# Performance work log

Hardware: AMD Instinct MI355X
Metric: run time of the kernel (lower is better)

Reference implementation:

```python
import jax, jax.numpy as jnp
import numpy as np

B, N, D = 256, 2048, 256

def setup_inputs() -> dict:
    key = jax.random.key(0)
    k1, k2, k3, k4 = jax.random.split(key, 4)
    feature = jax.random.normal(k1, (B, N, D), dtype=jnp.float32)
    pointer_hidden_state = jax.random.normal(k2, (B, D), dtype=jnp.float32)
    # learned params (match torch.randn init)
    v = jax.random.normal(k3, (1, 1, D), dtype=jnp.float32)
    W = jax.random.normal(k4, (1, D, 2 * D), dtype=jnp.float32)
    return {"feature": feature, "pointer_hidden_state": pointer_hidden_state, "v": v, "W": W}

def reference(feature, pointer_hidden_state, v, W):
    # hidden: concat(feature, broadcast hidden state) -> [B, N, 2D]
    b, n, d = feature.shape
    h = jnp.broadcast_to(pointer_hidden_state[:, None, :], (b, n, d))
    hidden = jnp.concatenate([feature, h], axis=2)            # [B, N, 2D]
    # W @ hidden^T fused as einsum: [D, 2D] x [B, N, 2D] -> [B, N, D]
    pre = jnp.tanh(jnp.einsum('de,bne->bnd', W[0], hidden))
    # v . pre -> [B, N]
    scores = jnp.einsum('d,bnd->bn', v[0, 0], pre)
    attns = jax.nn.softmax(scores, axis=1)[:, None, :]        # [B, 1, N]
    return attns
```

## Files before the change

kernel.cpp:

```cpp
#include <hip/hip_runtime.h>
#include <hip/hip_fp16.h>

typedef _Float16 f16;
typedef _Float16 f16x4 __attribute__((ext_vector_type(4)));
typedef _Float16 f16x8 __attribute__((ext_vector_type(8)));
typedef float f32x4 __attribute__((ext_vector_type(4)));

#define NCH 64
#define CHB 32768
#define PLB 16384
#define PSTRIDE 524288

#define BAR()     asm volatile("s_waitcnt lgkmcnt(0)\n\ts_barrier" ::: "memory")
#define WAITV_(N) asm volatile("s_waitcnt vmcnt(" #N ")" ::: "memory")
#define WAITV(N)  WAITV_(N)

__global__ void prep_w(const float* __restrict__ W, f16* __restrict__ wbuf) {
    int idx = blockIdx.x * 256 + threadIdx.x;
    int d = idx >> 8, k = idx & 255;
    float w = W[d * 512 + k];
    int ct   = d >> 4;
    int lane = (d & 15) | (((k >> 3) & 3) << 4);
    int ks   = k >> 5;
    int j    = k & 7;
    wbuf[(((ks * 16 + ct) * 64) + lane) * 8 + j] = (f16)w;
}

__global__ void prep_c(const float* __restrict__ W, const float* __restrict__ h,
                       float* __restrict__ c) {
    __shared__ float hs[256];
    int b = blockIdx.x, d = threadIdx.x;
    hs[d] = h[b * 256 + d];
    __syncthreads();
    const float4* w4 = (const float4*)(W + d * 512 + 256);
    const float4* h4 = (const float4*)hs;
    float acc = 0.f;
#pragma unroll 8
    for (int e = 0; e < 64; ++e) {
        float4 a = w4[e], bb = h4[e];
        acc += a.x * bb.x + a.y * bb.y + a.z * bb.z + a.w * bb.w;
    }
    c[b * 256 + d] = acc;
}

__global__ __launch_bounds__(512, 2)
void main_gemm(const float* __restrict__ feat, const f16* __restrict__ wbuf,
               const float* __restrict__ cb, const float* __restrict__ vvec,
               float* __restrict__ psc) {
    __shared__ __align__(16) char rawb[2 * CHB];
    __shared__ __align__(16) char plnb[2 * PLB];

    const int tid = threadIdx.x;
    const int w = tid >> 6;
    const int l = tid & 63;
    const int g = l >> 4;
    const int lr = l & 15;
    const int rh = w >> 2;
    const int cg = w & 3;
    const int b = blockIdx.x;

    f16x8 wf[4][8];
    {
        const f16x8* wp = (const f16x8*)wbuf;
#pragma unroll
        for (int ct = 0; ct < 4; ++ct) {
            int ctg = cg * 4 + ct;
#pragma unroll
            for (int ks = 0; ks < 8; ++ks)
                wf[ct][ks] = wp[(ks * 16 + ctg) * 64 + l];
        }
    }
    float c_[4], v_[4];
#pragma unroll
    for (int ct = 0; ct < 4; ++ct) {
        c_[ct] = cb[b * 256 + (cg * 4 + ct) * 16 + lr];
        v_[ct] = vvec[(cg * 4 + ct) * 16 + lr];
    }

    const char* tbb = (const char*)(feat + (size_t)b * 2048 * 256);

#define ISSUE(u)                                                                   \
    {                                                                              \
        const char* nb = tbb + (size_t)(u) * CHB;                                  \
        char* Q = rawb + ((u) & 1) * CHB;                                          \
        _Pragma("unroll")                                                          \
        for (int i = 0; i < 4; ++i)                                                \
            __builtin_amdgcn_global_load_lds(                                      \
                (const __attribute__((address_space(1))) void*)(nb + i * 8192 + tid * 16), \
                (__attribute__((address_space(3))) void*)(Q + i * 8192 + tid * 16),\
                16, 0, 0);                                                         \
    }

    const int ck0 = (tid & 63) * 4;
    int cvt_off[4];
#pragma unroll
    for (int r = 0; r < 4; ++r) {
        int row = r * 8 + w;
        cvt_off[r] = (((row * 512 + (ck0 & ~7) * 2) ^ ((row & 7) << 4)) +
                      ((ck0 & 4) << 1));
    }

#define CVT(u)                                                                     \
    {                                                                              \
        const char* rp = rawb + ((u) & 1) * CHB;                                   \
        char* hq = plnb + ((u) & 1) * PLB;                                         \
        _Pragma("unroll")                                                          \
        for (int r = 0; r < 4; ++r) {                                              \
            f32x4 x = *(const f32x4*)(rp + r * 8192 + tid * 16);                   \
            f16x4 hv = {(f16)x[0], (f16)x[1], (f16)x[2], (f16)x[3]};               \
            *(f16x4*)(hq + cvt_off[r]) = hv;                                       \
        }                                                                          \
    }

    const int arow = rh * 16 + lr;
    const int aswz = (arow & 7) << 4;

    ISSUE(0); ISSUE(1);
    WAITV(4);
    CVT(0);

    for (int t = 0; t < NCH; ++t) {
        BAR();
        if (t + 2 < NCH) ISSUE(t + 2);

        const char* hp = plnb + (t & 1) * PLB;
        f32x4 acc[4] = {};
#pragma unroll
        for (int ks = 0; ks < 8; ++ks) {
            int ao = (arow * 512 + ks * 64 + g * 16) ^ aswz;
            f16x8 ahi = *(const f16x8*)(hp + ao);
            acc[0] = __builtin_amdgcn_mfma_f32_16x16x32_f16(ahi, wf[0][ks], acc[0], 0, 0, 0);
            acc[1] = __builtin_amdgcn_mfma_f32_16x16x32_f16(ahi, wf[1][ks], acc[1], 0, 0, 0);
            acc[2] = __builtin_amdgcn_mfma_f32_16x16x32_f16(ahi, wf[2][ks], acc[2], 0, 0, 0);
            acc[3] = __builtin_amdgcn_mfma_f32_16x16x32_f16(ahi, wf[3][ks], acc[3], 0, 0, 0);
        }

        float s[4];
#pragma unroll
        for (int r = 0; r < 4; ++r) {
            float a = 0.f;
#pragma unroll
            for (int ct = 0; ct < 4; ++ct) {
                float x = acc[ct][r] + c_[ct];
                float tnh = 1.f - __fdividef(2.f, __expf(2.f * x) + 1.f);
                a += v_[ct] * tnh;
            }
            s[r] = a;
        }
#pragma unroll
        for (int m = 1; m < 16; m <<= 1) {
            s[0] += __shfl_xor(s[0], m, 64);
            s[1] += __shfl_xor(s[1], m, 64);
            s[2] += __shfl_xor(s[2], m, 64);
            s[3] += __shfl_xor(s[3], m, 64);
        }

        if (t < NCH - 2)      WAITV(4);
        else if (t == NCH - 2) WAITV(0);
        if (t + 1 < NCH) CVT(t + 1);

        if (lr == 0) {
            size_t rowg = (size_t)b * 2048 + t * 32 + rh * 16 + g * 4;
            float4 o = {s[0], s[1], s[2], s[3]};
            *(float4*)(psc + (size_t)cg * PSTRIDE + rowg) = o;
        }
    }
#undef ISSUE
#undef CVT
}

__global__ void softmax_k(const float* __restrict__ psc, float* __restrict__ out) {
    __shared__ float red[16];
    int b = blockIdx.x, tid = threadIdx.x;
    float sc[8];
    float m = -3.4e38f;
#pragma unroll
    for (int q = 0; q < 8; ++q) {
        size_t row = (size_t)b * 2048 + q * 256 + tid;
        sc[q] = (psc[row] + psc[PSTRIDE + row]) +
                (psc[2 * PSTRIDE + row] + psc[3 * PSTRIDE + row]);
        m = fmaxf(m, sc[q]);
    }
#pragma unroll
    for (int d = 1; d < 64; d <<= 1) m = fmaxf(m, __shfl_xor(m, d, 64));
    if ((tid & 63) == 0) red[tid >> 6] = m;
    __syncthreads();
    m = fmaxf(fmaxf(red[0], red[1]), fmaxf(red[2], red[3]));
    float e[8], sum = 0.f;
#pragma unroll
    for (int q = 0; q < 8; ++q) { e[q] = __expf(sc[q] - m); sum += e[q]; }
#pragma unroll
    for (int d = 1; d < 64; d <<= 1) sum += __shfl_xor(sum, d, 64);
    if ((tid & 63) == 0) red[8 + (tid >> 6)] = sum;
    __syncthreads();
    sum = (red[8] + red[9]) + (red[10] + red[11]);
    float inv = __fdividef(1.f, sum);
#pragma unroll
    for (int q = 0; q < 8; ++q)
        out[(size_t)b * 2048 + q * 256 + tid] = e[q] * inv;
}

extern "C" void kernel_launch(void* const* d_in, const int* in_sizes, int n_in,
                              void* d_out, int out_size, void* d_ws, size_t ws_size,
                              hipStream_t stream) {
    const float* feat = (const float*)d_in[0];
    const float* h    = (const float*)d_in[1];
    const float* v    = (const float*)d_in[2];
    const float* W    = (const float*)d_in[3];
    float* out = (float*)d_out;

    f16*   wbuf = (f16*)d_ws;
    float* cbuf = (float*)((char*)d_ws + 131072);
    float* psc  = (float*)((char*)d_ws + 524288);

    prep_w<<<256, 256, 0, stream>>>(W, wbuf);
    prep_c<<<256, 256, 0, stream>>>(W, h, cbuf);
    main_gemm<<<256, 512, 0, stream>>>(feat, wbuf, cbuf, v, psc);
    softmax_k<<<256, 256, 0, stream>>>(psc, out);
}
```

Before: 167.7 us.

## Software-pipeline tanh epilogue and fp16 conversion with MFMA chunk loop

Unrolls the chunk loop by two and double-buffers the accumulators in accA and accB. The tanh/v-dot epilogue and shuffle reduction of the previous chunk, plus the fp32-to-fp16 conversion of the next chunk, are interleaved between the MFMA k-steps of the current chunk. The goal is to hide the transcendental and LDS conversion latency behind matrix-core work. The cost is a second set of accumulators on a kernel that already holds a large register-resident W fragment, so spills or lower occupancy are possible. Score stores now lag one chunk, and the drain steps use adjusted vmcnt waits.

```diff
diff --git a/kernel.cpp b/kernel.cpp
--- a/kernel.cpp
+++ b/kernel.cpp
@@ -81,13 +81,13 @@
 
 #define ISSUE(u)                                                                   \
     {                                                                              \
-        const char* nb = tbb + (size_t)(u) * CHB;                                  \
-        char* Q = rawb + ((u) & 1) * CHB;                                          \
+        const char* nb_ = tbb + (size_t)(u) * CHB;                                 \
+        char* Q_ = rawb + ((u) & 1) * CHB;                                         \
         _Pragma("unroll")                                                          \
-        for (int i = 0; i < 4; ++i)                                                \
+        for (int i_ = 0; i_ < 4; ++i_)                                             \
             __builtin_amdgcn_global_load_lds(                                      \
-                (const __attribute__((address_space(1))) void*)(nb + i * 8192 + tid * 16), \
-                (__attribute__((address_space(3))) void*)(Q + i * 8192 + tid * 16),\
+                (const __attribute__((address_space(1))) void*)(nb_ + i_ * 8192 + tid * 16), \
+                (__attribute__((address_space(3))) void*)(Q_ + i_ * 8192 + tid * 16),\
                 16, 0, 0);                                                         \
     }
 
@@ -100,73 +100,96 @@
                       ((ck0 & 4) << 1));
     }
 
-#define CVT(u)                                                                     \
-    {                                                                              \
-        const char* rp = rawb + ((u) & 1) * CHB;                                   \
-        char* hq = plnb + ((u) & 1) * PLB;                                         \
-        _Pragma("unroll")                                                          \
-        for (int r = 0; r < 4; ++r) {                                              \
-            f32x4 x = *(const f32x4*)(rp + r * 8192 + tid * 16);                   \
-            f16x4 hv = {(f16)x[0], (f16)x[1], (f16)x[2], (f16)x[3]};               \
-            *(f16x4*)(hq + cvt_off[r]) = hv;                                       \
-        }                                                                          \
+#define CVTR(U, R)                                                                 \
+    {                                                                              \
+        const char* rp_ = rawb + ((U) & 1) * CHB;                                  \
+        char* hq_ = plnb + ((U) & 1) * PLB;                                        \
+        f32x4 x_ = *(const f32x4*)(rp_ + (R) * 8192 + tid * 16);                   \
+        f16x4 hv_ = {(f16)x_[0], (f16)x_[1], (f16)x_[2], (f16)x_[3]};              \
+        *(f16x4*)(hq_ + cvt_off[R]) = hv_;                                         \
     }
 
     const int arow = rh * 16 + lr;
     const int aswz = (arow & 7) << 4;
 
+#define KS(KSI, ACC)                                                               \
+    {                                                                              \
+        int ao_ = (arow * 512 + (KSI) * 64 + g * 16) ^ aswz;                       \
+        f16x8 ah_ = *(const f16x8*)(hp_ + ao_);                                    \
+        ACC[0] = __builtin_amdgcn_mfma_f32_16x16x32_f16(ah_, wf[0][KSI], ACC[0], 0, 0, 0); \
+        ACC[1] = __builtin_amdgcn_mfma_f32_16x16x32_f16(ah_, wf[1][KSI], ACC[1], 0, 0, 0); \
+        ACC[2] = __builtin_amdgcn_mfma_f32_16x16x32_f16(ah_, wf[2][KSI], ACC[2], 0, 0, 0); \
+        ACC[3] = __builtin_amdgcn_mfma_f32_16x16x32_f16(ah_, wf[3][KSI], ACC[3], 0, 0, 0); \
+    }
+
+#define EPIS(ACCP, R, SV)                                                          \
+    {                                                                              \
+        float a_ = 0.f;                                                            \
+        _Pragma("unroll")                                                          \
+        for (int ct_ = 0; ct_ < 4; ++ct_) {                                        \
+            float x_ = ACCP[ct_][R] + c_[ct_];                                     \
+            float t_ = 1.f - __fdividef(2.f, __expf(2.f * x_) + 1.f);              \
+            a_ += v_[ct_] * t_;                                                    \
+        }                                                                          \
+        a_ += __shfl_xor(a_, 1, 64);                                               \
+        a_ += __shfl_xor(a_, 2, 64);                                               \
+        a_ += __shfl_xor(a_, 4, 64);                                               \
+        a_ += __shfl_xor(a_, 8, 64);                                               \
+        SV = a_;                                                                   \
+    }
+
+#define STEP(T, ACC, ACCP, DOISS, WS, DOCVT)                                       \
+    {                                                                              \
+        BAR();                                                                     \
+        if (DOISS) ISSUE((T) + 2);                                                 \
+        WS;                                                                        \
+        const char* hp_ = plnb + ((T) & 1) * PLB;                                  \
+        ACC[0] = zf; ACC[1] = zf; ACC[2] = zf; ACC[3] = zf;                        \
+        float sA_, sB_, sC_, sD_;                                                  \
+        KS(0, ACC) if (DOCVT) CVTR((T) + 1, 0)                                     \
+        KS(1, ACC) EPIS(ACCP, 0, sA_)                                              \
+        KS(2, ACC) if (DOCVT) CVTR((T) + 1, 1)                                     \
+        KS(3, ACC) EPIS(ACCP, 1, sB_)                                              \
+        KS(4, ACC) if (DOCVT) CVTR((T) + 1, 2)                                     \
+        KS(5, ACC) EPIS(ACCP, 2, sC_)                                              \
+        KS(6, ACC) if (DOCVT) CVTR((T) + 1, 3)                                     \
+        KS(7, ACC) EPIS(ACCP, 3, sD_)                                              \
+        if ((T) > 0 && lr == 0) {                                                  \
+            size_t rowg = (size_t)b * 2048 + (size_t)((T) - 1) * 32 + rh * 16 + g * 4; \
+            float4 o_ = {sA_, sB_, sC_, sD_};                                      \
+            *(float4*)(psc + (size_t)cg * PSTRIDE + rowg) = o_;                    \
+        }                                                                          \
+    }
+
+    const f32x4 zf = {0.f, 0.f, 0.f, 0.f};
+    f32x4 accA[4] = {zf, zf, zf, zf};
+    f32x4 accB[4] = {zf, zf, zf, zf};
+
     ISSUE(0); ISSUE(1);
     WAITV(4);
-    CVT(0);
-
-    for (int t = 0; t < NCH; ++t) {
-        BAR();
-        if (t + 2 < NCH) ISSUE(t + 2);
-
-        const char* hp = plnb + (t & 1) * PLB;
-        f32x4 acc[4] = {};
-#pragma unroll
-        for (int ks = 0; ks < 8; ++ks) {
-            int ao = (arow * 512 + ks * 64 + g * 16) ^ aswz;
-            f16x8 ahi = *(const f16x8*)(hp + ao);
-            acc[0] = __builtin_amdgcn_mfma_f32_16x16x32_f16(ahi, wf[0][ks], acc[0], 0, 0, 0);
-            acc[1] = __builtin_amdgcn_mfma_f32_16x16x32_f16(ahi, wf[1][ks], acc[1], 0, 0, 0);
-            acc[2] = __builtin_amdgcn_mfma_f32_16x16x32_f16(ahi, wf[2][ks], acc[2], 0, 0, 0);
-            acc[3] = __builtin_amdgcn_mfma_f32_16x16x32_f16(ahi, wf[3][ks], acc[3], 0, 0, 0);
+    CVTR(0, 0) CVTR(0, 1) CVTR(0, 2) CVTR(0, 3)
+
+    for (int tt = 0; tt < 31; ++tt) {
+        const int t0 = 2 * tt;
+        STEP(t0,     accA, accB, 1, WAITV(4), 1)
+        STEP(t0 + 1, accB, accA, 1, WAITV(4), 1)
+    }
+    STEP(62, accA, accB, 0, WAITV(1), 1)
+    STEP(63, accB, accA, 0, ((void)0), 0)
+    {
+        float s0_, s1_, s2_, s3_;
+        EPIS(accB, 0, s0_) EPIS(accB, 1, s1_) EPIS(accB, 2, s2_) EPIS(accB, 3, s3_)
+        if (lr == 0) {
+            size_t rowg = (size_t)b * 2048 + (size_t)63 * 32 + rh * 16 + g * 4;
+            float4 o_ = {s0_, s1_, s2_, s3_};
+            *(float4*)(psc + (size_t)cg * PSTRIDE + rowg) = o_;
         }
-
-        float s[4];
-#pragma unroll
-        for (int r = 0; r < 4; ++r) {
-            float a = 0.f;
-#pragma unroll
-            for (int ct = 0; ct < 4; ++ct) {
-                float x = acc[ct][r] + c_[ct];
-                float tnh = 1.f - __fdividef(2.f, __expf(2.f * x) + 1.f);
-                a += v_[ct] * tnh;
-            }
-            s[r] = a;
-        }
-#pragma unroll
-        for (int m = 1; m < 16; m <<= 1) {
-            s[0] += __shfl_xor(s[0], m, 64);
-            s[1] += __shfl_xor(s[1], m, 64);
-            s[2] += __shfl_xor(s[2], m, 64);
-            s[3] += __shfl_xor(s[3], m, 64);
-        }
-
-        if (t < NCH - 2)      WAITV(4);
-        else if (t == NCH - 2) WAITV(0);
-        if (t + 1 < NCH) CVT(t + 1);
-
-        if (lr == 0) {
-            size_t rowg = (size_t)b * 2048 + t * 32 + rh * 16 + g * 4;
-            float4 o = {s[0], s[1], s[2], s[3]};
-            *(float4*)(psc + (size_t)cg * PSTRIDE + rowg) = o;
-        }
     }
 #undef ISSUE
-#undef CVT
+#undef CVTR
+#undef KS
+#undef EPIS
+#undef STEP
 }
 
 __global__ void softmax_k(const float* __restrict__ psc, float* __restrict__ out) {
```

Result: slower. 174.8 us (+4.2%).

## Load feature chunks into registers instead of async global-to-LDS staging

Applied to the files above, without the earlier changes.

Replaces the double-buffered global_load_lds staging of raw fp32 feature chunks with direct global loads into registers, converted to fp16 and written to the LDS tile. This removes the 64KB raw LDS buffer and the extra LDS read pass, which could improve occupancy. In exchange, prefetch depth drops from two chunks ahead to one and register pressure rises, so more memory latency may be exposed.

```diff
diff --git a/kernel.cpp b/kernel.cpp
--- a/kernel.cpp
+++ b/kernel.cpp
@@ -47,7 +47,6 @@
 void main_gemm(const float* __restrict__ feat, const f16* __restrict__ wbuf,
                const float* __restrict__ cb, const float* __restrict__ vvec,
                float* __restrict__ psc) {
-    __shared__ __align__(16) char rawb[2 * CHB];
     __shared__ __align__(16) char plnb[2 * PLB];
 
     const int tid = threadIdx.x;
@@ -79,16 +78,14 @@
 
     const char* tbb = (const char*)(feat + (size_t)b * 2048 * 256);
 
-#define ISSUE(u)                                                                   \
+    f32x4 st[4];
+#define LOADC(u)                                                                   \
     {                                                                              \
-        const char* nb = tbb + (size_t)(u) * CHB;                                  \
-        char* Q = rawb + ((u) & 1) * CHB;                                          \
-        _Pragma("unroll")                                                          \
-        for (int i = 0; i < 4; ++i)                                                \
-            __builtin_amdgcn_global_load_lds(                                      \
-                (const __attribute__((address_space(1))) void*)(nb + i * 8192 + tid * 16), \
-                (__attribute__((address_space(3))) void*)(Q + i * 8192 + tid * 16),\
-                16, 0, 0);                                                         \
+        const f32x4* sp_ = (const f32x4*)(tbb + (size_t)(u) * CHB + tid * 16);     \
+        st[0] = sp_[0];                                                            \
+        st[1] = sp_[512];                                                          \
+        st[2] = sp_[1024];                                                         \
+        st[3] = sp_[1536];                                                         \
     }
 
     const int ck0 = (tid & 63) * 4;
@@ -100,28 +97,26 @@
                       ((ck0 & 4) << 1));
     }
 
-#define CVT(u)                                                                     \
+#define CVTW(u)                                                                    \
     {                                                                              \
-        const char* rp = rawb + ((u) & 1) * CHB;                                   \
-        char* hq = plnb + ((u) & 1) * PLB;                                         \
+        char* hq_ = plnb + ((u) & 1) * PLB;                                        \
         _Pragma("unroll")                                                          \
         for (int r = 0; r < 4; ++r) {                                              \
-            f32x4 x = *(const f32x4*)(rp + r * 8192 + tid * 16);                   \
-            f16x4 hv = {(f16)x[0], (f16)x[1], (f16)x[2], (f16)x[3]};               \
-            *(f16x4*)(hq + cvt_off[r]) = hv;                                       \
+            f16x4 hv_ = {(f16)st[r][0], (f16)st[r][1], (f16)st[r][2], (f16)st[r][3]}; \
+            *(f16x4*)(hq_ + cvt_off[r]) = hv_;                                     \
         }                                                                          \
     }
 
     const int arow = rh * 16 + lr;
     const int aswz = (arow & 7) << 4;
 
-    ISSUE(0); ISSUE(1);
-    WAITV(4);
-    CVT(0);
+    LOADC(0);
+    WAITV(0);
+    CVTW(0);
 
     for (int t = 0; t < NCH; ++t) {
         BAR();
-        if (t + 2 < NCH) ISSUE(t + 2);
+        if (t + 1 < NCH) LOADC(t + 1);
 
         const char* hp = plnb + (t & 1) * PLB;
         f32x4 acc[4] = {};
@@ -155,18 +150,19 @@
             s[3] += __shfl_xor(s[3], m, 64);
         }
 
-        if (t < NCH - 2)      WAITV(4);
-        else if (t == NCH - 2) WAITV(0);
-        if (t + 1 < NCH) CVT(t + 1);
+        if (t + 1 < NCH) {
+            WAITV(0);
+            CVTW(t + 1);
+        }
 
         if (lr == 0) {
-            size_t rowg = (size_t)b * 2048 + t * 32 + rh * 16 + g * 4;
+            size_t rowg = (size_t)b * 2048 + (size_t)t * 32 + rh * 16 + g * 4;
             float4 o = {s[0], s[1], s[2], s[3]};
             *(float4*)(psc + (size_t)cg * PSTRIDE + rowg) = o;
         }
     }
-#undef ISSUE
-#undef CVT
+#undef LOADC
+#undef CVTW
 }
 
 __global__ void softmax_k(const float* __restrict__ psc, float* __restrict__ out) {
```

Result: slower. 213.2 us (+27.2%).

## Split GEMM tile across 16 waves with two column tiles each

Applied to the files above, without the earlier changes.

The main GEMM block grows from 512 to 1024 threads. Each wave now computes 2 of the 16-wide output column tiles instead of 4, which halves the W fragments, accumulators and tanh work it holds. The global-to-LDS loads and the fp16 conversion are spread over the larger thread count, and the softmax kernel now sums 8 partial score arrays instead of 4. The aim is more waves per CU to hide streaming-load latency, at the cost of more LDS A-fragment reads, more partial-score traffic and losing the 2-blocks-per-CU launch bound.

```diff
diff --git a/kernel.cpp b/kernel.cpp
--- a/kernel.cpp
+++ b/kernel.cpp
@@ -43,7 +43,7 @@
     c[b * 256 + d] = acc;
 }
 
-__global__ __launch_bounds__(512, 2)
+__global__ __launch_bounds__(1024)
 void main_gemm(const float* __restrict__ feat, const f16* __restrict__ wbuf,
                const float* __restrict__ cb, const float* __restrict__ vvec,
                float* __restrict__ psc) {
@@ -55,60 +55,60 @@
     const int l = tid & 63;
     const int g = l >> 4;
     const int lr = l & 15;
-    const int rh = w >> 2;
-    const int cg = w & 3;
+    const int rh = w & 1;
+    const int cg = w >> 1;
     const int b = blockIdx.x;
 
-    f16x8 wf[4][8];
+    f16x8 wf[2][8];
     {
         const f16x8* wp = (const f16x8*)wbuf;
 #pragma unroll
-        for (int ct = 0; ct < 4; ++ct) {
-            int ctg = cg * 4 + ct;
+        for (int ct = 0; ct < 2; ++ct) {
+            int ctg = cg * 2 + ct;
 #pragma unroll
             for (int ks = 0; ks < 8; ++ks)
                 wf[ct][ks] = wp[(ks * 16 + ctg) * 64 + l];
         }
     }
-    float c_[4], v_[4];
-#pragma unroll
-    for (int ct = 0; ct < 4; ++ct) {
-        c_[ct] = cb[b * 256 + (cg * 4 + ct) * 16 + lr];
-        v_[ct] = vvec[(cg * 4 + ct) * 16 + lr];
+    float c_[2], v_[2];
+#pragma unroll
+    for (int ct = 0; ct < 2; ++ct) {
+        c_[ct] = cb[b * 256 + (cg * 2 + ct) * 16 + lr];
+        v_[ct] = vvec[(cg * 2 + ct) * 16 + lr];
     }
 
     const char* tbb = (const char*)(feat + (size_t)b * 2048 * 256);
 
 #define ISSUE(u)                                                                   \
     {                                                                              \
-        const char* nb = tbb + (size_t)(u) * CHB;                                  \
-        char* Q = rawb + ((u) & 1) * CHB;                                          \
+        const char* nb_ = tbb + (size_t)(u) * CHB;                                 \
+        char* Q_ = rawb + ((u) & 1) * CHB;                                         \
         _Pragma("unroll")                                                          \
-        for (int i = 0; i < 4; ++i)                                                \
+        for (int i_ = 0; i_ < 2; ++i_)                                             \
             __builtin_amdgcn_global_load_lds(                                      \
-                (const __attribute__((address_space(1))) void*)(nb + i * 8192 + tid * 16), \
-                (__attribute__((address_space(3))) void*)(Q + i * 8192 + tid * 16),\
+                (const __attribute__((address_space(1))) void*)(nb_ + i_ * 16384 + tid * 16), \
+                (__attribute__((address_space(3))) void*)(Q_ + i_ * 16384 + tid * 16),\
                 16, 0, 0);                                                         \
     }
 
     const int ck0 = (tid & 63) * 4;
-    int cvt_off[4];
-#pragma unroll
-    for (int r = 0; r < 4; ++r) {
-        int row = r * 8 + w;
+    int cvt_off[2];
+#pragma unroll
+    for (int r = 0; r < 2; ++r) {
+        int row = r * 16 + (tid >> 6);
         cvt_off[r] = (((row * 512 + (ck0 & ~7) * 2) ^ ((row & 7) << 4)) +
                       ((ck0 & 4) << 1));
     }
 
 #define CVT(u)                                                                     \
     {                                                                              \
-        const char* rp = rawb + ((u) & 1) * CHB;                                   \
-        char* hq = plnb + ((u) & 1) * PLB;                                         \
+        const char* rp_ = rawb + ((u) & 1) * CHB;                                  \
+        char* hq_ = plnb + ((u) & 1) * PLB;                                        \
         _Pragma("unroll")                                                          \
-        for (int r = 0; r < 4; ++r) {                                              \
-            f32x4 x = *(const f32x4*)(rp + r * 8192 + tid * 16);                   \
-            f16x4 hv = {(f16)x[0], (f16)x[1], (f16)x[2], (f16)x[3]};               \
-            *(f16x4*)(hq + cvt_off[r]) = hv;                                       \
+        for (int r = 0; r < 2; ++r) {                                              \
+            f32x4 x_ = *(const f32x4*)(rp_ + r * 16384 + tid * 16);                \
+            f16x4 hv_ = {(f16)x_[0], (f16)x_[1], (f16)x_[2], (f16)x_[3]};          \
+            *(f16x4*)(hq_ + cvt_off[r]) = hv_;                                     \
         }                                                                          \
     }
 
@@ -116,7 +116,7 @@
     const int aswz = (arow & 7) << 4;
 
     ISSUE(0); ISSUE(1);
-    WAITV(4);
+    WAITV(2);
     CVT(0);
 
     for (int t = 0; t < NCH; ++t) {
@@ -124,28 +124,23 @@
         if (t + 2 < NCH) ISSUE(t + 2);
 
         const char* hp = plnb + (t & 1) * PLB;
-        f32x4 acc[4] = {};
+        f32x4 acc[2] = {};
 #pragma unroll
         for (int ks = 0; ks < 8; ++ks) {
             int ao = (arow * 512 + ks * 64 + g * 16) ^ aswz;
             f16x8 ahi = *(const f16x8*)(hp + ao);
             acc[0] = __builtin_amdgcn_mfma_f32_16x16x32_f16(ahi, wf[0][ks], acc[0], 0, 0, 0);
             acc[1] = __builtin_amdgcn_mfma_f32_16x16x32_f16(ahi, wf[1][ks], acc[1], 0, 0, 0);
-            acc[2] = __builtin_amdgcn_mfma_f32_16x16x32_f16(ahi, wf[2][ks], acc[2], 0, 0, 0);
-            acc[3] = __builtin_amdgcn_mfma_f32_16x16x32_f16(ahi, wf[3][ks], acc[3], 0, 0, 0);
         }
 
         float s[4];
 #pragma unroll
         for (int r = 0; r < 4; ++r) {
-            float a = 0.f;
-#pragma unroll
-            for (int ct = 0; ct < 4; ++ct) {
-                float x = acc[ct][r] + c_[ct];
-                float tnh = 1.f - __fdividef(2.f, __expf(2.f * x) + 1.f);
-                a += v_[ct] * tnh;
-            }
-            s[r] = a;
+            float x0 = acc[0][r] + c_[0];
+            float x1 = acc[1][r] + c_[1];
+            float t0 = 1.f - __fdividef(2.f, __expf(2.f * x0) + 1.f);
+            float t1 = 1.f - __fdividef(2.f, __expf(2.f * x1) + 1.f);
+            s[r] = v_[0] * t0 + v_[1] * t1;
         }
 #pragma unroll
         for (int m = 1; m < 16; m <<= 1) {
@@ -155,12 +150,12 @@
             s[3] += __shfl_xor(s[3], m, 64);
         }
 
-        if (t < NCH - 2)      WAITV(4);
+        if (t < NCH - 2)      WAITV(2);
         else if (t == NCH - 2) WAITV(0);
         if (t + 1 < NCH) CVT(t + 1);
 
         if (lr == 0) {
-            size_t rowg = (size_t)b * 2048 + t * 32 + rh * 16 + g * 4;
+            size_t rowg = (size_t)b * 2048 + (size_t)t * 32 + rh * 16 + g * 4;
             float4 o = {s[0], s[1], s[2], s[3]};
             *(float4*)(psc + (size_t)cg * PSTRIDE + rowg) = o;
         }
@@ -177,8 +172,11 @@
 #pragma unroll
     for (int q = 0; q < 8; ++q) {
         size_t row = (size_t)b * 2048 + q * 256 + tid;
-        sc[q] = (psc[row] + psc[PSTRIDE + row]) +
-                (psc[2 * PSTRIDE + row] + psc[3 * PSTRIDE + row]);
+        float a0 = psc[row] + psc[PSTRIDE + row];
+        float a1 = psc[2 * PSTRIDE + row] + psc[3 * PSTRIDE + row];
+        float a2 = psc[4 * PSTRIDE + row] + psc[5 * PSTRIDE + row];
+        float a3 = psc[6 * PSTRIDE + row] + psc[7 * PSTRIDE + row];
+        sc[q] = (a0 + a1) + (a2 + a3);
         m = fmaxf(m, sc[q]);
     }
 #pragma unroll
@@ -215,6 +213,6 @@
 
     prep_w<<<256, 256, 0, stream>>>(W, wbuf);
     prep_c<<<256, 256, 0, stream>>>(W, h, cbuf);
-    main_gemm<<<256, 512, 0, stream>>>(feat, wbuf, cbuf, v, psc);
+    main_gemm<<<256, 1024, 0, stream>>>(feat, wbuf, cbuf, v, psc);
     softmax_k<<<256, 256, 0, stream>>>(psc, out);
 }
```

Measured after the change: 178.1 us. 6.2% more time.
